# Performance work log

Hardware: AMD Instinct MI355X
Metric: run time of the kernel (lower is better)

Reference implementation:

```python
import jax, jax.numpy as jnp
import numpy as np

SCALE = 8.0  # sqrt(head_dim=64)
B, H, S, D = 2, 16, 2048, 64


def setup_inputs() -> dict:
    key = jax.random.key(0)
    kq, kk, kv = jax.random.split(key, 3)
    query = jax.random.normal(kq, (B, H, S, D), dtype=jnp.float32)
    key_t = jax.random.normal(kk, (B, H, S, D), dtype=jnp.float32)
    value = jax.random.normal(kv, (B, H, S, D), dtype=jnp.float32)
    # causal target mask (B, 1, S, S); 0 = masked
    mask = jnp.broadcast_to(jnp.tril(jnp.ones((S, S), dtype=jnp.int32)), (B, 1, S, S))
    return {"query": query, "key": key_t, "value": value, "mask": mask}


def reference(query, key, value, mask):
    # scores: (B, H, S, S)
    scores = jnp.einsum("bhqd,bhkd->bhqk", query, key) / SCALE
    scores = jnp.where(mask == 0, -jnp.inf, scores)
    attn = jax.nn.softmax(scores, axis=-1)  # dropout_rate=0.0 -> identity
    return jnp.einsum("bhqk,bhkd->bhqd", attn, value)
```

## Files before the change

### kernel.cpp

```cpp
#include <hip/hip_runtime.h>
#include <hip/hip_bf16.h>


#define S_ 2048
#define D_ 64
#define NBH 32

typedef __bf16 bf16x8 __attribute__((ext_vector_type(8)));
typedef float f32x16 __attribute__((ext_vector_type(16)));
typedef unsigned short u16x4 __attribute__((ext_vector_type(4)));
typedef unsigned short u16x8 __attribute__((ext_vector_type(8)));
typedef unsigned int u32;
typedef u32 u32x4 __attribute__((ext_vector_type(4)));

static __device__ __forceinline__ unsigned short bfb(float f) {
    return __builtin_bit_cast(unsigned short, (__bf16)f);
}
static __device__ __forceinline__ u32 pk2(float lo, float hi) {
    return (u32)bfb(lo) | ((u32)bfb(hi) << 16);
}

__global__ __launch_bounds__(256)
void prep_kv(const float* __restrict__ K, const float* __restrict__ V,
             unsigned short* __restrict__ Kbf, unsigned short* __restrict__ Vt) {
    const int bh = blockIdx.x >> 5;
    const int kvbase = (blockIdx.x & 31) << 6;

    const float* Ks = K + (size_t)bh * S_ * D_ + (size_t)kvbase * D_;
    unsigned short* Kd = Kbf + (size_t)bh * S_ * D_ + (size_t)kvbase * D_;
    #pragma unroll
    for (int i = 0; i < 4; ++i) {
        const int p = i * 256 + threadIdx.x;
        float4 x = reinterpret_cast<const float4*>(Ks)[p];
        u16x4 o = { bfb(x.x), bfb(x.y), bfb(x.z), bfb(x.w) };
        reinterpret_cast<u16x4*>(Kd)[p] = o;
    }

    __shared__ float Vl[64][65];
    const float* Vb = V + (size_t)bh * S_ * D_ + (size_t)kvbase * D_;
    #pragma unroll
    for (int i = 0; i < 4; ++i) {
        const int flat = i * 1024 + threadIdx.x * 4;
        const int kv = flat >> 6, d = flat & 63;
        float4 x = *reinterpret_cast<const float4*>(Vb + kv * D_ + d);
        Vl[kv][d] = x.x; Vl[kv][d + 1] = x.y; Vl[kv][d + 2] = x.z; Vl[kv][d + 3] = x.w;
    }
    __syncthreads();
    unsigned short* Vo = Vt + (size_t)bh * D_ * S_;
    #pragma unroll
    for (int i = 0; i < 2; ++i) {
        const int p = i * 256 + threadIdx.x;
        const int d = p >> 3, c = p & 7;
        u16x8 o;
        #pragma unroll
        for (int j = 0; j < 8; ++j) o[j] = bfb(Vl[c * 8 + j][d]);
        *reinterpret_cast<u16x8*>(Vo + d * S_ + kvbase + c * 8) = o;
    }
}

#define MFMA32(a, b, c) __builtin_amdgcn_mfma_f32_32x32x16_bf16((a), (b), (c), 0, 0, 0)

__global__ __launch_bounds__(256, 2)
void attn_fwd6(const float* __restrict__ Q, const unsigned short* __restrict__ Kbf,
               const unsigned short* __restrict__ Vtbf, float* __restrict__ O) {
    const int tid  = threadIdx.x;
    const int wq   = tid >> 6;
    const int lane = tid & 63;
    const int lq   = lane & 31;
    const int hi   = lane >> 5;

    const int bid = blockIdx.x;
    const int bh  = bid & 31;
    const int jb  = 15 - (bid >> 5);
    const int q0w = jb * 128 + wq * 32;

    const int nkv_b = 2 * jb + 2;
    const int nkv_w = 2 * jb + 1 + (wq >> 1);

    const unsigned short* Kg = Kbf  + (size_t)bh * S_ * D_;
    const unsigned short* Vg = Vtbf + (size_t)bh * D_ * S_;

    __shared__ __align__(16) unsigned short Kl[2][4096];
    __shared__ __align__(16) unsigned short Vl[2][4096];

    const float qscale = 0.18033688011112042f;
    bf16x8 qf[4];
    {
        const float* qsrc = Q + ((size_t)bh * S_ + q0w + lq) * D_;
        #pragma unroll
        for (int ks = 0; ks < 4; ++ks) {
            const float* p = qsrc + ks * 16 + hi * 8;
            float4 x = *reinterpret_cast<const float4*>(p);
            float4 y = *reinterpret_cast<const float4*>(p + 4);
            union { unsigned short u[8]; bf16x8 v; } t;
            t.u[0] = bfb(x.x * qscale); t.u[1] = bfb(x.y * qscale);
            t.u[2] = bfb(x.z * qscale); t.u[3] = bfb(x.w * qscale);
            t.u[4] = bfb(y.x * qscale); t.u[5] = bfb(y.y * qscale);
            t.u[6] = bfb(y.z * qscale); t.u[7] = bfb(y.w * qscale);
            qf[ks] = t.v;
        }
    }

    bf16x8 ones;
    #pragma unroll
    for (int i = 0; i < 8; ++i) ones[i] = (__bf16)1.0f;

    const unsigned short* kSrc[2];
    const unsigned short* vSrc[2];
    #pragma unroll
    for (int i = 0; i < 2; ++i) {
        const int p = i * 256 + tid, row = p >> 3;
        const int sc = (p & 7) ^ (row & 7);
        kSrc[i] = Kg + row * 64 + sc * 8;
        vSrc[i] = Vg + (size_t)row * S_ + sc * 8;
    }
    auto stage = [&](int buf, int t) {
        #pragma unroll
        for (int i = 0; i < 2; ++i) {
            const int p = i * 256 + tid;
            __builtin_amdgcn_global_load_lds(
                (const __attribute__((address_space(1))) void*)(kSrc[i] + t * 4096),
                (__attribute__((address_space(3))) void*)&Kl[buf][p * 8], 16, 0, 0);
            __builtin_amdgcn_global_load_lds(
                (const __attribute__((address_space(1))) void*)(vSrc[i] + t * 64),
                (__attribute__((address_space(3))) void*)&Vl[buf][p * 8], 16, 0, 0);
        }
    };

    f32x16 oa0, oa1, ssum;
    #pragma unroll
    for (int r = 0; r < 16; ++r) { oa0[r] = 0.f; oa1[r] = 0.f; ssum[r] = 0.f; }
    float m_ = -__builtin_inff();

    stage(0, 0);
    __syncthreads();

    for (int t = 0; t < nkv_b; ++t) {
        if (t + 1 < nkv_b) stage((t + 1) & 1, t + 1);
        if (t < nkv_w) {
            const unsigned short* Kb_ = Kl[t & 1];
            const unsigned short* Vb_ = Vl[t & 1];

            f32x16 s0, s1;
            #pragma unroll
            for (int r = 0; r < 16; ++r) { s0[r] = 0.f; s1[r] = 0.f; }
            __builtin_amdgcn_s_setprio(1);
            #pragma unroll
            for (int ks = 0; ks < 4; ++ks) {
                const int cc = 2 * ks + hi;
                bf16x8 k0 = *reinterpret_cast<const bf16x8*>(
                    &Kb_[((lq)*8      + (cc ^ (lq & 7))) * 8]);
                bf16x8 k1 = *reinterpret_cast<const bf16x8*>(
                    &Kb_[((32 + lq)*8 + (cc ^ (lq & 7))) * 8]);
                s0 = MFMA32(k0, qf[ks], s0);
                s1 = MFMA32(k1, qf[ks], s1);
            }
            __builtin_amdgcn_s_setprio(0);

            if (t == nkv_w - 1) {
                const int qg = q0w + lq - t * 64;
                #pragma unroll
                for (int r = 0; r < 16; ++r) {
                    const int kv0 = (r & 3) + 8 * (r >> 2) + 4 * hi;
                    if (kv0 > qg)      s0[r] = -__builtin_inff();
                    if (kv0 + 32 > qg) s1[r] = -__builtin_inff();
                }
            }

            float v = s0[0];
            #pragma unroll
            for (int r = 1; r < 16; ++r) v = fmaxf(v, s0[r]);
            #pragma unroll
            for (int r = 0; r < 16; ++r) v = fmaxf(v, s1[r]);
            v = fmaxf(v, __shfl_xor(v, 32));

            if (__any(v > m_ + 8.0f ? 1 : 0)) {
                const float mn = fmaxf(m_, v);
                const float al = __builtin_amdgcn_exp2f(m_ - mn);
                m_ = mn;
                ssum[0] *= al;
                #pragma unroll
                for (int r = 0; r < 16; ++r) { oa0[r] *= al; oa1[r] *= al; }
            }
            #pragma unroll
            for (int r = 0; r < 16; ++r) {
                s0[r] = __builtin_amdgcn_exp2f(s0[r] - m_);
                s1[r] = __builtin_amdgcn_exp2f(s1[r] - m_);
            }

            u32 c0[4][2], c1[4][2];
            #pragma unroll
            for (int tq = 0; tq < 4; ++tq) {
                c0[tq][0] = pk2(s0[4*tq+0], s0[4*tq+1]);
                c0[tq][1] = pk2(s0[4*tq+2], s0[4*tq+3]);
                c1[tq][0] = pk2(s1[4*tq+0], s1[4*tq+1]);
                c1[tq][1] = pk2(s1[4*tq+2], s1[4*tq+3]);
            }

            __builtin_amdgcn_s_setprio(1);
#define PVSTEP(KS, C, TL) { \
            u32 a0 = C[TL][0], a1 = C[TL][1], b0 = C[TL+1][0], b1 = C[TL+1][1]; \
            asm volatile("v_permlane32_swap_b32 %0, %1" : "+v"(a0), "+v"(b0)); \
            asm volatile("v_permlane32_swap_b32 %0, %1" : "+v"(a1), "+v"(b1)); \
            u32x4 w = { a0, a1, b0, b1 }; \
            bf16x8 pf = __builtin_bit_cast(bf16x8, w); \
            const int cc = 2*(KS) + hi; \
            bf16x8 v0 = *reinterpret_cast<const bf16x8*>( \
                &Vb_[((lq)*8      + (cc ^ (lq & 7))) * 8]); \
            bf16x8 v1 = *reinterpret_cast<const bf16x8*>( \
                &Vb_[((32 + lq)*8 + (cc ^ (lq & 7))) * 8]); \
            oa0 = MFMA32(v0, pf, oa0); \
            oa1 = MFMA32(v1, pf, oa1); \
            ssum = MFMA32(ones, pf, ssum); }
            PVSTEP(0, c0, 0) PVSTEP(1, c0, 2) PVSTEP(2, c1, 0) PVSTEP(3, c1, 2)
#undef PVSTEP
            __builtin_amdgcn_s_setprio(0);
        }
        __syncthreads();
    }

    const float inv = 1.0f / ssum[0];
    float* Ob = O + ((size_t)bh * S_ + q0w + lq) * D_;
    #pragma unroll
    for (int g = 0; g < 4; ++g) {
        float4 o0 = { oa0[4*g+0]*inv, oa0[4*g+1]*inv, oa0[4*g+2]*inv, oa0[4*g+3]*inv };
        *reinterpret_cast<float4*>(&Ob[8*g + 4*hi]) = o0;
        float4 o1 = { oa1[4*g+0]*inv, oa1[4*g+1]*inv, oa1[4*g+2]*inv, oa1[4*g+3]*inv };
        *reinterpret_cast<float4*>(&Ob[32 + 8*g + 4*hi]) = o1;
    }
}

extern "C" void kernel_launch(void* const* d_in, const int* in_sizes, int n_in,
                              void* d_out, int out_size, void* d_ws, size_t ws_size,
                              hipStream_t stream) {
    const float* Q = (const float*)d_in[0];
    const float* K = (const float*)d_in[1];
    const float* V = (const float*)d_in[2];
    float* O = (float*)d_out;

    unsigned short* Kbf = (unsigned short*)d_ws;
    unsigned short* Vt  = Kbf + (size_t)NBH * S_ * D_;

    hipLaunchKernelGGL(prep_kv,   dim3(1024), dim3(256), 0, stream, K, V, Kbf, Vt);
    hipLaunchKernelGGL(attn_fwd6, dim3(512),  dim3(256), 0, stream, Q, Kbf, Vt, O);
}
```

Before: 152.5 us.

## Split causal KV range across two blocks and merge partial outputs

Each query block's causal KV range is split into two halves processed by separate blocks (1024 blocks instead of 512). Each half writes unnormalized partial outputs plus its running max and sum. A new combine kernel then merges the halves with log-sum-exp weights. The aim is to shorten the critical path set by the longest diagonal blocks and to balance load across CUs. The cost is extra global traffic for the partial outputs, the stats and an extra launch. The original kernel remains as a fallback when the workspace is too small.

```diff
diff --git a/kernel.cpp b/kernel.cpp
--- a/kernel.cpp
+++ b/kernel.cpp
@@ -60,77 +60,211 @@
 
 #define MFMA32(a, b, c) __builtin_amdgcn_mfma_f32_32x32x16_bf16((a), (b), (c), 0, 0, 0)
 
+#define TILE_BODY(Kb_, Vb_, doMask, qg_expr)                                     \
+    {                                                                            \
+        f32x16 s0, s1;                                                           \
+        _Pragma("unroll")                                                        \
+        for (int r = 0; r < 16; ++r) { s0[r] = 0.f; s1[r] = 0.f; }               \
+        __builtin_amdgcn_s_setprio(1);                                           \
+        _Pragma("unroll")                                                        \
+        for (int ks = 0; ks < 4; ++ks) {                                         \
+            const int cc = 2 * ks + hi;                                          \
+            bf16x8 k0 = *reinterpret_cast<const bf16x8*>(                        \
+                &Kb_[((lq)*8      + (cc ^ (lq & 7))) * 8]);                      \
+            bf16x8 k1 = *reinterpret_cast<const bf16x8*>(                        \
+                &Kb_[((32 + lq)*8 + (cc ^ (lq & 7))) * 8]);                      \
+            s0 = MFMA32(k0, qf[ks], s0);                                         \
+            s1 = MFMA32(k1, qf[ks], s1);                                         \
+        }                                                                        \
+        __builtin_amdgcn_s_setprio(0);                                           \
+        if (doMask) {                                                            \
+            const int qg = (qg_expr);                                            \
+            _Pragma("unroll")                                                    \
+            for (int r = 0; r < 16; ++r) {                                       \
+                const int kv0 = (r & 3) + 8 * (r >> 2) + 4 * hi;                 \
+                if (kv0 > qg)      s0[r] = -__builtin_inff();                    \
+                if (kv0 + 32 > qg) s1[r] = -__builtin_inff();                    \
+            }                                                                    \
+        }                                                                        \
+        float v = s0[0];                                                         \
+        _Pragma("unroll")                                                        \
+        for (int r = 1; r < 16; ++r) v = fmaxf(v, s0[r]);                        \
+        _Pragma("unroll")                                                        \
+        for (int r = 0; r < 16; ++r) v = fmaxf(v, s1[r]);                        \
+        v = fmaxf(v, __shfl_xor(v, 32));                                         \
+        if (__any(v > m_ + 8.0f ? 1 : 0)) {                                      \
+            const float mn = fmaxf(m_, v);                                       \
+            const float al = __builtin_amdgcn_exp2f(m_ - mn);                    \
+            m_ = mn;                                                             \
+            ssum[0] *= al;                                                       \
+            _Pragma("unroll")                                                    \
+            for (int r = 0; r < 16; ++r) { oa0[r] *= al; oa1[r] *= al; }         \
+        }                                                                        \
+        _Pragma("unroll")                                                        \
+        for (int r = 0; r < 16; ++r) {                                           \
+            s0[r] = __builtin_amdgcn_exp2f(s0[r] - m_);                          \
+            s1[r] = __builtin_amdgcn_exp2f(s1[r] - m_);                          \
+        }                                                                        \
+        u32 c0[4][2], c1[4][2];                                                  \
+        _Pragma("unroll")                                                        \
+        for (int tq = 0; tq < 4; ++tq) {                                         \
+            c0[tq][0] = pk2(s0[4*tq+0], s0[4*tq+1]);                             \
+            c0[tq][1] = pk2(s0[4*tq+2], s0[4*tq+3]);                             \
+            c1[tq][0] = pk2(s1[4*tq+0], s1[4*tq+1]);                             \
+            c1[tq][1] = pk2(s1[4*tq+2], s1[4*tq+3]);                             \
+        }                                                                        \
+        __builtin_amdgcn_s_setprio(1);                                           \
+        PVSTEP(0, c0, 0) PVSTEP(1, c0, 2) PVSTEP(2, c1, 0) PVSTEP(3, c1, 2)      \
+        __builtin_amdgcn_s_setprio(0);                                           \
+    }
+
+#define PVSTEP(KS, C, TL) {                                                      \
+    u32 a0 = C[TL][0], a1 = C[TL][1], b0 = C[TL+1][0], b1 = C[TL+1][1];          \
+    asm volatile("v_permlane32_swap_b32 %0, %1" : "+v"(a0), "+v"(b0));           \
+    asm volatile("v_permlane32_swap_b32 %0, %1" : "+v"(a1), "+v"(b1));           \
+    u32x4 w = { a0, a1, b0, b1 };                                                \
+    bf16x8 pf = __builtin_bit_cast(bf16x8, w);                                   \
+    const int cc = 2*(KS) + hi;                                                  \
+    bf16x8 v0 = *reinterpret_cast<const bf16x8*>(                                \
+        &Vb_[((lq)*8      + (cc ^ (lq & 7))) * 8]);                              \
+    bf16x8 v1 = *reinterpret_cast<const bf16x8*>(                                \
+        &Vb_[((32 + lq)*8 + (cc ^ (lq & 7))) * 8]);                              \
+    oa0 = MFMA32(v0, pf, oa0);                                                   \
+    oa1 = MFMA32(v1, pf, oa1);                                                   \
+    ssum = MFMA32(ones, pf, ssum); }
+
+#define ATTN_PROLOGUE(Q0W_EXPR)                                                  \
+    const int tid  = threadIdx.x;                                                \
+    const int wq   = tid >> 6;                                                   \
+    const int lane = tid & 63;                                                   \
+    const int lq   = lane & 31;                                                  \
+    const int hi   = lane >> 5;                                                  \
+    const int q0w  = (Q0W_EXPR);                                                 \
+    const unsigned short* Kg = Kbf  + (size_t)bh * S_ * D_;                      \
+    const unsigned short* Vg = Vtbf + (size_t)bh * D_ * S_;                      \
+    const float qscale = 0.18033688011112042f;                                   \
+    bf16x8 qf[4];                                                                \
+    {                                                                            \
+        const float* qsrc = Q + ((size_t)bh * S_ + q0w + lq) * D_;               \
+        _Pragma("unroll")                                                        \
+        for (int ks = 0; ks < 4; ++ks) {                                         \
+            const float* p = qsrc + ks * 16 + hi * 8;                            \
+            float4 x = *reinterpret_cast<const float4*>(p);                      \
+            float4 y = *reinterpret_cast<const float4*>(p + 4);                  \
+            union { unsigned short u[8]; bf16x8 v; } tt;                         \
+            tt.u[0] = bfb(x.x * qscale); tt.u[1] = bfb(x.y * qscale);            \
+            tt.u[2] = bfb(x.z * qscale); tt.u[3] = bfb(x.w * qscale);            \
+            tt.u[4] = bfb(y.x * qscale); tt.u[5] = bfb(y.y * qscale);            \
+            tt.u[6] = bfb(y.z * qscale); tt.u[7] = bfb(y.w * qscale);            \
+            qf[ks] = tt.v;                                                       \
+        }                                                                        \
+    }                                                                            \
+    bf16x8 ones;                                                                 \
+    _Pragma("unroll")                                                            \
+    for (int i = 0; i < 8; ++i) ones[i] = (__bf16)1.0f;                          \
+    const unsigned short* kSrc[2];                                               \
+    const unsigned short* vSrc[2];                                               \
+    _Pragma("unroll")                                                            \
+    for (int i = 0; i < 2; ++i) {                                                \
+        const int p = i * 256 + tid, row = p >> 3;                               \
+        const int sc = (p & 7) ^ (row & 7);                                      \
+        kSrc[i] = Kg + row * 64 + sc * 8;                                        \
+        vSrc[i] = Vg + (size_t)row * S_ + sc * 8;                                \
+    }                                                                            \
+    auto stage = [&](int buf, int t) {                                           \
+        _Pragma("unroll")                                                        \
+        for (int i = 0; i < 2; ++i) {                                            \
+            const int p = i * 256 + tid;                                         \
+            __builtin_amdgcn_global_load_lds(                                    \
+                (const __attribute__((address_space(1))) void*)(kSrc[i] + t * 4096), \
+                (__attribute__((address_space(3))) void*)&Kl[buf][p * 8], 16, 0, 0); \
+            __builtin_amdgcn_global_load_lds(                                    \
+                (const __attribute__((address_space(1))) void*)(vSrc[i] + t * 64),   \
+                (__attribute__((address_space(3))) void*)&Vl[buf][p * 8], 16, 0, 0); \
+        }                                                                        \
+    };                                                                           \
+    f32x16 oa0, oa1, ssum;                                                       \
+    _Pragma("unroll")                                                            \
+    for (int r = 0; r < 16; ++r) { oa0[r] = 0.f; oa1[r] = 0.f; ssum[r] = 0.f; }  \
+    float m_ = -__builtin_inff();
+
+__global__ __launch_bounds__(256, 2)
+void attn_split(const float* __restrict__ Q, const unsigned short* __restrict__ Kbf,
+                const unsigned short* __restrict__ Vtbf,
+                float* __restrict__ OA, float* __restrict__ OB,
+                float* __restrict__ stats) {
+    const int bid  = blockIdx.x;
+    const int jb   = 15 - (bid >> 6);
+    const int half = (bid >> 5) & 1;
+    const int bh   = bid & 31;
+
+    __shared__ __align__(16) unsigned short Kl[2][4096];
+    __shared__ __align__(16) unsigned short Vl[2][4096];
+
+    ATTN_PROLOGUE(jb * 128 + wq * 32)
+
+    const int t0   = half ? (jb + 1) : 0;
+    const int tEnd = half ? (2 * jb + 2) : (jb + 1);
+    const int nkv_w = 2 * jb + 1 + (wq >> 1);
+
+    stage(t0 & 1, t0);
+    __syncthreads();
+
+    for (int t = t0; t < tEnd; ++t) {
+        if (t + 1 < tEnd) stage((t + 1) & 1, t + 1);
+        if (t < nkv_w) {
+            const unsigned short* Kb_ = Kl[t & 1];
+            const unsigned short* Vb_ = Vl[t & 1];
+            TILE_BODY(Kb_, Vb_, (t == nkv_w - 1), q0w + lq - t * 64)
+        }
+        __syncthreads();
+    }
+
+    float* dst = (half ? OB : OA) + ((size_t)bh * S_ + q0w + lq) * D_;
+    #pragma unroll
+    for (int g = 0; g < 4; ++g) {
+        float4 o0 = { oa0[4*g+0], oa0[4*g+1], oa0[4*g+2], oa0[4*g+3] };
+        *reinterpret_cast<float4*>(&dst[8*g + 4*hi]) = o0;
+        float4 o1 = { oa1[4*g+0], oa1[4*g+1], oa1[4*g+2], oa1[4*g+3] };
+        *reinterpret_cast<float4*>(&dst[32 + 8*g + 4*hi]) = o1;
+    }
+    if (hi == 0) {
+        float* st = stats + (((size_t)bh << 11) + q0w + lq) * 4 + (half ? 2 : 0);
+        st[0] = m_;
+        st[1] = ssum[0];
+    }
+}
+
+__global__ __launch_bounds__(256)
+void combine(float* __restrict__ OA, const float* __restrict__ OB,
+             const float4* __restrict__ stats) {
+    const int p = blockIdx.x * 256 + threadIdx.x;
+    const float4 s = stats[p >> 4];
+    const float m  = fmaxf(s.x, s.z);
+    const float wA = __builtin_amdgcn_exp2f(s.x - m);
+    const float wB = __builtin_amdgcn_exp2f(s.z - m);
+    const float inv = 1.0f / (s.y * wA + s.w * wB);
+    float4 a = reinterpret_cast<float4*>(OA)[p];
+    float4 b = reinterpret_cast<const float4*>(OB)[p];
+    float4 o = { (a.x * wA + b.x * wB) * inv, (a.y * wA + b.y * wB) * inv,
+                 (a.z * wA + b.z * wB) * inv, (a.w * wA + b.w * wB) * inv };
+    reinterpret_cast<float4*>(OA)[p] = o;
+}
+
 __global__ __launch_bounds__(256, 2)
 void attn_fwd6(const float* __restrict__ Q, const unsigned short* __restrict__ Kbf,
                const unsigned short* __restrict__ Vtbf, float* __restrict__ O) {
-    const int tid  = threadIdx.x;
-    const int wq   = tid >> 6;
-    const int lane = tid & 63;
-    const int lq   = lane & 31;
-    const int hi   = lane >> 5;
-
     const int bid = blockIdx.x;
     const int bh  = bid & 31;
     const int jb  = 15 - (bid >> 5);
-    const int q0w = jb * 128 + wq * 32;
+
+    __shared__ __align__(16) unsigned short Kl[2][4096];
+    __shared__ __align__(16) unsigned short Vl[2][4096];
+
+    ATTN_PROLOGUE(jb * 128 + wq * 32)
 
     const int nkv_b = 2 * jb + 2;
     const int nkv_w = 2 * jb + 1 + (wq >> 1);
-
-    const unsigned short* Kg = Kbf  + (size_t)bh * S_ * D_;
-    const unsigned short* Vg = Vtbf + (size_t)bh * D_ * S_;
-
-    __shared__ __align__(16) unsigned short Kl[2][4096];
-    __shared__ __align__(16) unsigned short Vl[2][4096];
-
-    const float qscale = 0.18033688011112042f;
-    bf16x8 qf[4];
-    {
-        const float* qsrc = Q + ((size_t)bh * S_ + q0w + lq) * D_;
-        #pragma unroll
-        for (int ks = 0; ks < 4; ++ks) {
-            const float* p = qsrc + ks * 16 + hi * 8;
-            float4 x = *reinterpret_cast<const float4*>(p);
-            float4 y = *reinterpret_cast<const float4*>(p + 4);
-            union { unsigned short u[8]; bf16x8 v; } t;
-            t.u[0] = bfb(x.x * qscale); t.u[1] = bfb(x.y * qscale);
-            t.u[2] = bfb(x.z * qscale); t.u[3] = bfb(x.w * qscale);
-            t.u[4] = bfb(y.x * qscale); t.u[5] = bfb(y.y * qscale);
-            t.u[6] = bfb(y.z * qscale); t.u[7] = bfb(y.w * qscale);
-            qf[ks] = t.v;
-        }
-    }
-
-    bf16x8 ones;
-    #pragma unroll
-    for (int i = 0; i < 8; ++i) ones[i] = (__bf16)1.0f;
-
-    const unsigned short* kSrc[2];
-    const unsigned short* vSrc[2];
-    #pragma unroll
-    for (int i = 0; i < 2; ++i) {
-        const int p = i * 256 + tid, row = p >> 3;
-        const int sc = (p & 7) ^ (row & 7);
-        kSrc[i] = Kg + row * 64 + sc * 8;
-        vSrc[i] = Vg + (size_t)row * S_ + sc * 8;
-    }
-    auto stage = [&](int buf, int t) {
-        #pragma unroll
-        for (int i = 0; i < 2; ++i) {
-            const int p = i * 256 + tid;
-            __builtin_amdgcn_global_load_lds(
-                (const __attribute__((address_space(1))) void*)(kSrc[i] + t * 4096),
-                (__attribute__((address_space(3))) void*)&Kl[buf][p * 8], 16, 0, 0);
-            __builtin_amdgcn_global_load_lds(
-                (const __attribute__((address_space(1))) void*)(vSrc[i] + t * 64),
-                (__attribute__((address_space(3))) void*)&Vl[buf][p * 8], 16, 0, 0);
-        }
-    };
-
-    f32x16 oa0, oa1, ssum;
-    #pragma unroll
-    for (int r = 0; r < 16; ++r) { oa0[r] = 0.f; oa1[r] = 0.f; ssum[r] = 0.f; }
-    float m_ = -__builtin_inff();
 
     stage(0, 0);
     __syncthreads();
@@ -140,81 +274,7 @@
         if (t < nkv_w) {
             const unsigned short* Kb_ = Kl[t & 1];
             const unsigned short* Vb_ = Vl[t & 1];
-
-            f32x16 s0, s1;
-            #pragma unroll
-            for (int r = 0; r < 16; ++r) { s0[r] = 0.f; s1[r] = 0.f; }
-            __builtin_amdgcn_s_setprio(1);
-            #pragma unroll
-            for (int ks = 0; ks < 4; ++ks) {
-                const int cc = 2 * ks + hi;
-                bf16x8 k0 = *reinterpret_cast<const bf16x8*>(
-                    &Kb_[((lq)*8      + (cc ^ (lq & 7))) * 8]);
-                bf16x8 k1 = *reinterpret_cast<const bf16x8*>(
-                    &Kb_[((32 + lq)*8 + (cc ^ (lq & 7))) * 8]);
-                s0 = MFMA32(k0, qf[ks], s0);
-                s1 = MFMA32(k1, qf[ks], s1);
-            }
-            __builtin_amdgcn_s_setprio(0);
-
-            if (t == nkv_w - 1) {
-                const int qg = q0w + lq - t * 64;
-                #pragma unroll
-                for (int r = 0; r < 16; ++r) {
-                    const int kv0 = (r & 3) + 8 * (r >> 2) + 4 * hi;
-                    if (kv0 > qg)      s0[r] = -__builtin_inff();
-                    if (kv0 + 32 > qg) s1[r] = -__builtin_inff();
-                }
-            }
-
-            float v = s0[0];
-            #pragma unroll
-            for (int r = 1; r < 16; ++r) v = fmaxf(v, s0[r]);
-            #pragma unroll
-            for (int r = 0; r < 16; ++r) v = fmaxf(v, s1[r]);
-            v = fmaxf(v, __shfl_xor(v, 32));
-
-            if (__any(v > m_ + 8.0f ? 1 : 0)) {
-                const float mn = fmaxf(m_, v);
-                const float al = __builtin_amdgcn_exp2f(m_ - mn);
-                m_ = mn;
-                ssum[0] *= al;
-                #pragma unroll
-                for (int r = 0; r < 16; ++r) { oa0[r] *= al; oa1[r] *= al; }
-            }
-            #pragma unroll
-            for (int r = 0; r < 16; ++r) {
-                s0[r] = __builtin_amdgcn_exp2f(s0[r] - m_);
-                s1[r] = __builtin_amdgcn_exp2f(s1[r] - m_);
-            }
-
-            u32 c0[4][2], c1[4][2];
-            #pragma unroll
-            for (int tq = 0; tq < 4; ++tq) {
-                c0[tq][0] = pk2(s0[4*tq+0], s0[4*tq+1]);
-                c0[tq][1] = pk2(s0[4*tq+2], s0[4*tq+3]);
-                c1[tq][0] = pk2(s1[4*tq+0], s1[4*tq+1]);
-                c1[tq][1] = pk2(s1[4*tq+2], s1[4*tq+3]);
-            }
-
-            __builtin_amdgcn_s_setprio(1);
-#define PVSTEP(KS, C, TL) { \
-            u32 a0 = C[TL][0], a1 = C[TL][1], b0 = C[TL+1][0], b1 = C[TL+1][1]; \
-            asm volatile("v_permlane32_swap_b32 %0, %1" : "+v"(a0), "+v"(b0)); \
-            asm volatile("v_permlane32_swap_b32 %0, %1" : "+v"(a1), "+v"(b1)); \
-            u32x4 w = { a0, a1, b0, b1 }; \
-            bf16x8 pf = __builtin_bit_cast(bf16x8, w); \
-            const int cc = 2*(KS) + hi; \
-            bf16x8 v0 = *reinterpret_cast<const bf16x8*>( \
-                &Vb_[((lq)*8      + (cc ^ (lq & 7))) * 8]); \
-            bf16x8 v1 = *reinterpret_cast<const bf16x8*>( \
-                &Vb_[((32 + lq)*8 + (cc ^ (lq & 7))) * 8]); \
-            oa0 = MFMA32(v0, pf, oa0); \
-            oa1 = MFMA32(v1, pf, oa1); \
-            ssum = MFMA32(ones, pf, ssum); }
-            PVSTEP(0, c0, 0) PVSTEP(1, c0, 2) PVSTEP(2, c1, 0) PVSTEP(3, c1, 2)
-#undef PVSTEP
-            __builtin_amdgcn_s_setprio(0);
+            TILE_BODY(Kb_, Vb_, (t == nkv_w - 1), q0w + lq - t * 64)
         }
         __syncthreads();
     }
@@ -241,6 +301,20 @@
     unsigned short* Kbf = (unsigned short*)d_ws;
     unsigned short* Vt  = Kbf + (size_t)NBH * S_ * D_;
 
-    hipLaunchKernelGGL(prep_kv,   dim3(1024), dim3(256), 0, stream, K, V, Kbf, Vt);
-    hipLaunchKernelGGL(attn_fwd6, dim3(512),  dim3(256), 0, stream, Q, Kbf, Vt, O);
-}
+    hipLaunchKernelGGL(prep_kv, dim3(1024), dim3(256), 0, stream, K, V, Kbf, Vt);
+
+    const size_t needed = (size_t)NBH * S_ * D_ * 2 * 2
+                        + (size_t)NBH * S_ * D_ * 4
+                        + (size_t)NBH * S_ * 16;
+    if (ws_size >= needed) {
+        float* OB    = (float*)(Vt + (size_t)NBH * S_ * D_);
+        float* stats = OB + (size_t)NBH * S_ * D_;
+        hipLaunchKernelGGL(attn_split, dim3(1024), dim3(256), 24576, stream,
+                           Q, Kbf, Vt, O, OB, stats);
+        hipLaunchKernelGGL(combine, dim3(4096), dim3(256), 0, stream,
+                           O, OB, (const float4*)stats);
+    } else {
+        hipLaunchKernelGGL(attn_fwd6, dim3(512), dim3(256), 0, stream,
+                           Q, Kbf, Vt, O);
+    }
+}
```

New measurement: 153.0 us. No clear change (+0.3%).

## Pre-swizzle K/V into MFMA fragment layout and load per-wave from global, dropping LDS

Applied to the files above, without the earlier changes.

The prep kernel now writes K and V in bf16 directly in the per-lane MFMA operand order, so each wave in the attention kernel loads its fragments straight from global memory into registers. This removes LDS staging and block-wide barriers. Each wave becomes an independent 32-row query strip, with causal load balancing done by pairing long and short strips across waves. The row sum is now computed with VALU reductions instead of an extra ones-MFMA. The cost is that each wave re-reads K/V from global or L2 without sharing across the block, which raises L2 traffic and register pressure.

```diff
diff --git a/kernel.cpp b/kernel.cpp
--- a/kernel.cpp
+++ b/kernel.cpp
@@ -8,7 +8,6 @@
 
 typedef __bf16 bf16x8 __attribute__((ext_vector_type(8)));
 typedef float f32x16 __attribute__((ext_vector_type(16)));
-typedef unsigned short u16x4 __attribute__((ext_vector_type(4)));
 typedef unsigned short u16x8 __attribute__((ext_vector_type(8)));
 typedef unsigned int u32;
 typedef u32 u32x4 __attribute__((ext_vector_type(4)));
@@ -21,67 +20,81 @@
 }
 
 __global__ __launch_bounds__(256)
-void prep_kv(const float* __restrict__ K, const float* __restrict__ V,
-             unsigned short* __restrict__ Kbf, unsigned short* __restrict__ Vt) {
+void prep_frag(const float* __restrict__ K, const float* __restrict__ V,
+               unsigned short* __restrict__ Kf, unsigned short* __restrict__ Vf) {
     const int bh = blockIdx.x >> 5;
-    const int kvbase = (blockIdx.x & 31) << 6;
-
-    const float* Ks = K + (size_t)bh * S_ * D_ + (size_t)kvbase * D_;
-    unsigned short* Kd = Kbf + (size_t)bh * S_ * D_ + (size_t)kvbase * D_;
-    #pragma unroll
-    for (int i = 0; i < 4; ++i) {
-        const int p = i * 256 + threadIdx.x;
-        float4 x = reinterpret_cast<const float4*>(Ks)[p];
-        u16x4 o = { bfb(x.x), bfb(x.y), bfb(x.z), bfb(x.w) };
-        reinterpret_cast<u16x4*>(Kd)[p] = o;
-    }
-
-    __shared__ float Vl[64][65];
-    const float* Vb = V + (size_t)bh * S_ * D_ + (size_t)kvbase * D_;
+    const int t  = blockIdx.x & 31;
+    __shared__ float Ka[64][65];
+    __shared__ float Va[64][65];
+    const float* Ks = K + ((size_t)bh * S_ + t * 64) * D_;
+    const float* Vs = V + ((size_t)bh * S_ + t * 64) * D_;
     #pragma unroll
     for (int i = 0; i < 4; ++i) {
         const int flat = i * 1024 + threadIdx.x * 4;
-        const int kv = flat >> 6, d = flat & 63;
-        float4 x = *reinterpret_cast<const float4*>(Vb + kv * D_ + d);
-        Vl[kv][d] = x.x; Vl[kv][d + 1] = x.y; Vl[kv][d + 2] = x.z; Vl[kv][d + 3] = x.w;
+        const int s = flat >> 6, d = flat & 63;
+        float4 kx = *reinterpret_cast<const float4*>(Ks + s * D_ + d);
+        Ka[s][d] = kx.x; Ka[s][d+1] = kx.y; Ka[s][d+2] = kx.z; Ka[s][d+3] = kx.w;
+        float4 vx = *reinterpret_cast<const float4*>(Vs + s * D_ + d);
+        Va[s][d] = vx.x; Va[s][d+1] = vx.y; Va[s][d+2] = vx.z; Va[s][d+3] = vx.w;
     }
     __syncthreads();
-    unsigned short* Vo = Vt + (size_t)bh * D_ * S_;
+    const size_t tb = ((size_t)bh * 32 + t) * 512;
     #pragma unroll
     for (int i = 0; i < 2; ++i) {
-        const int p = i * 256 + threadIdx.x;
-        const int d = p >> 3, c = p & 7;
-        u16x8 o;
-        #pragma unroll
-        for (int j = 0; j < 8; ++j) o[j] = bfb(Vl[c * 8 + j][d]);
-        *reinterpret_cast<u16x8*>(Vo + d * S_ + kvbase + c * 8) = o;
+        const int u  = i * 256 + threadIdx.x;
+        const int h  = u >> 8, ks = (u >> 6) & 3, h2 = (u >> 5) & 1, l2 = u & 31;
+        const int d0 = 8 * (2 * ks + h2);
+        u16x8 ok, ov;
+        #pragma unroll
+        for (int j = 0; j < 8; ++j) {
+            ok[j] = bfb(Ka[h * 32 + l2][d0 + j]);
+            ov[j] = bfb(Va[d0 + j][h * 32 + l2]);
+        }
+        *reinterpret_cast<u16x8*>(Kf + (tb + u) * 8) = ok;
+        *reinterpret_cast<u16x8*>(Vf + (tb + u) * 8) = ov;
     }
 }
 
 #define MFMA32(a, b, c) __builtin_amdgcn_mfma_f32_32x32x16_bf16((a), (b), (c), 0, 0, 0)
 
+#define LOADF(DST, BASE, T) { \
+    const unsigned short* fb_ = (BASE) + (size_t)(T) * 4096 + lane * 8; \
+    DST[0] = *reinterpret_cast<const bf16x8*>(fb_); \
+    DST[1] = *reinterpret_cast<const bf16x8*>(fb_ + 512); \
+    DST[2] = *reinterpret_cast<const bf16x8*>(fb_ + 1024); \
+    DST[3] = *reinterpret_cast<const bf16x8*>(fb_ + 1536); \
+    DST[4] = *reinterpret_cast<const bf16x8*>(fb_ + 2048); \
+    DST[5] = *reinterpret_cast<const bf16x8*>(fb_ + 2560); \
+    DST[6] = *reinterpret_cast<const bf16x8*>(fb_ + 3072); \
+    DST[7] = *reinterpret_cast<const bf16x8*>(fb_ + 3584); }
+
+#define PVSTEP(KS, C, TL) { \
+    u32 a0 = C[TL][0], a1 = C[TL][1], b0 = C[TL+1][0], b1 = C[TL+1][1]; \
+    asm volatile("v_permlane32_swap_b32 %0, %1" : "+v"(a0), "+v"(b0)); \
+    asm volatile("v_permlane32_swap_b32 %0, %1" : "+v"(a1), "+v"(b1)); \
+    u32x4 w = { a0, a1, b0, b1 }; \
+    bf16x8 pf = __builtin_bit_cast(bf16x8, w); \
+    oa0 = MFMA32(vA[KS],     pf, oa0); \
+    oa1 = MFMA32(vA[4 + KS], pf, oa1); }
+
 __global__ __launch_bounds__(256, 2)
-void attn_fwd6(const float* __restrict__ Q, const unsigned short* __restrict__ Kbf,
-               const unsigned short* __restrict__ Vtbf, float* __restrict__ O) {
+void attn_frag(const float* __restrict__ Q, const unsigned short* __restrict__ Kf,
+               const unsigned short* __restrict__ Vf, float* __restrict__ O) {
     const int tid  = threadIdx.x;
     const int wq   = tid >> 6;
     const int lane = tid & 63;
     const int lq   = lane & 31;
     const int hi   = lane >> 5;
 
-    const int bid = blockIdx.x;
-    const int bh  = bid & 31;
-    const int jb  = 15 - (bid >> 5);
-    const int q0w = jb * 128 + wq * 32;
-
-    const int nkv_b = 2 * jb + 2;
-    const int nkv_w = 2 * jb + 1 + (wq >> 1);
-
-    const unsigned short* Kg = Kbf  + (size_t)bh * S_ * D_;
-    const unsigned short* Vg = Vtbf + (size_t)bh * D_ * S_;
-
-    __shared__ __align__(16) unsigned short Kl[2][4096];
-    __shared__ __align__(16) unsigned short Vl[2][4096];
+    const int wid = blockIdx.x * 4 + wq;
+    int qs, bh;
+    if (wid < 1024) { qs = 63 - (wid >> 5); bh = wid & 31; }
+    else            { qs = (wid - 1024) >> 5; bh = (wid - 1024) & 31; }
+    const int q0w = qs * 32;
+    const int nt  = (qs >> 1) + 1;
+
+    const unsigned short* Kg = Kf + (size_t)bh * 131072;
+    const unsigned short* Vg = Vf + (size_t)bh * 131072;
 
     const float qscale = 0.18033688011112042f;
     bf16x8 qf[4];
@@ -92,134 +105,98 @@
             const float* p = qsrc + ks * 16 + hi * 8;
             float4 x = *reinterpret_cast<const float4*>(p);
             float4 y = *reinterpret_cast<const float4*>(p + 4);
-            union { unsigned short u[8]; bf16x8 v; } t;
-            t.u[0] = bfb(x.x * qscale); t.u[1] = bfb(x.y * qscale);
-            t.u[2] = bfb(x.z * qscale); t.u[3] = bfb(x.w * qscale);
-            t.u[4] = bfb(y.x * qscale); t.u[5] = bfb(y.y * qscale);
-            t.u[6] = bfb(y.z * qscale); t.u[7] = bfb(y.w * qscale);
-            qf[ks] = t.v;
-        }
-    }
-
-    bf16x8 ones;
-    #pragma unroll
-    for (int i = 0; i < 8; ++i) ones[i] = (__bf16)1.0f;
-
-    const unsigned short* kSrc[2];
-    const unsigned short* vSrc[2];
-    #pragma unroll
-    for (int i = 0; i < 2; ++i) {
-        const int p = i * 256 + tid, row = p >> 3;
-        const int sc = (p & 7) ^ (row & 7);
-        kSrc[i] = Kg + row * 64 + sc * 8;
-        vSrc[i] = Vg + (size_t)row * S_ + sc * 8;
-    }
-    auto stage = [&](int buf, int t) {
-        #pragma unroll
-        for (int i = 0; i < 2; ++i) {
-            const int p = i * 256 + tid;
-            __builtin_amdgcn_global_load_lds(
-                (const __attribute__((address_space(1))) void*)(kSrc[i] + t * 4096),
-                (__attribute__((address_space(3))) void*)&Kl[buf][p * 8], 16, 0, 0);
-            __builtin_amdgcn_global_load_lds(
-                (const __attribute__((address_space(1))) void*)(vSrc[i] + t * 64),
-                (__attribute__((address_space(3))) void*)&Vl[buf][p * 8], 16, 0, 0);
-        }
-    };
-
-    f32x16 oa0, oa1, ssum;
-    #pragma unroll
-    for (int r = 0; r < 16; ++r) { oa0[r] = 0.f; oa1[r] = 0.f; ssum[r] = 0.f; }
-    float m_ = -__builtin_inff();
-
-    stage(0, 0);
-    __syncthreads();
-
-    for (int t = 0; t < nkv_b; ++t) {
-        if (t + 1 < nkv_b) stage((t + 1) & 1, t + 1);
-        if (t < nkv_w) {
-            const unsigned short* Kb_ = Kl[t & 1];
-            const unsigned short* Vb_ = Vl[t & 1];
-
-            f32x16 s0, s1;
-            #pragma unroll
-            for (int r = 0; r < 16; ++r) { s0[r] = 0.f; s1[r] = 0.f; }
-            __builtin_amdgcn_s_setprio(1);
-            #pragma unroll
-            for (int ks = 0; ks < 4; ++ks) {
-                const int cc = 2 * ks + hi;
-                bf16x8 k0 = *reinterpret_cast<const bf16x8*>(
-                    &Kb_[((lq)*8      + (cc ^ (lq & 7))) * 8]);
-                bf16x8 k1 = *reinterpret_cast<const bf16x8*>(
-                    &Kb_[((32 + lq)*8 + (cc ^ (lq & 7))) * 8]);
-                s0 = MFMA32(k0, qf[ks], s0);
-                s1 = MFMA32(k1, qf[ks], s1);
+            union { unsigned short u[8]; bf16x8 v; } tt;
+            tt.u[0] = bfb(x.x * qscale); tt.u[1] = bfb(x.y * qscale);
+            tt.u[2] = bfb(x.z * qscale); tt.u[3] = bfb(x.w * qscale);
+            tt.u[4] = bfb(y.x * qscale); tt.u[5] = bfb(y.y * qscale);
+            tt.u[6] = bfb(y.z * qscale); tt.u[7] = bfb(y.w * qscale);
+            qf[ks] = tt.v;
+        }
+    }
+
+    f32x16 oa0, oa1;
+    #pragma unroll
+    for (int r = 0; r < 16; ++r) { oa0[r] = 0.f; oa1[r] = 0.f; }
+    float m_ = -__builtin_inff(), l_ = 0.f;
+
+    bf16x8 kA[8], vA[8];
+    LOADF(kA, Kg, 0)
+    LOADF(vA, Vg, 0)
+
+    for (int t = 0; t < nt; ++t) {
+        const int tn = (t + 1 < 32) ? (t + 1) : 31;
+
+        f32x16 s0, s1;
+        #pragma unroll
+        for (int r = 0; r < 16; ++r) { s0[r] = 0.f; s1[r] = 0.f; }
+        __builtin_amdgcn_s_setprio(1);
+        #pragma unroll
+        for (int ks = 0; ks < 4; ++ks) {
+            s0 = MFMA32(kA[ks],     qf[ks], s0);
+            s1 = MFMA32(kA[4 + ks], qf[ks], s1);
+        }
+        __builtin_amdgcn_s_setprio(0);
+
+        LOADF(kA, Kg, tn)
+
+        if (t == nt - 1) {
+            const int qg = q0w + lq - t * 64;
+            #pragma unroll
+            for (int r = 0; r < 16; ++r) {
+                const int kv0 = (r & 3) + 8 * (r >> 2) + 4 * hi;
+                if (kv0 > qg)      s0[r] = -__builtin_inff();
+                if (kv0 + 32 > qg) s1[r] = -__builtin_inff();
             }
-            __builtin_amdgcn_s_setprio(0);
-
-            if (t == nkv_w - 1) {
-                const int qg = q0w + lq - t * 64;
-                #pragma unroll
-                for (int r = 0; r < 16; ++r) {
-                    const int kv0 = (r & 3) + 8 * (r >> 2) + 4 * hi;
-                    if (kv0 > qg)      s0[r] = -__builtin_inff();
-                    if (kv0 + 32 > qg) s1[r] = -__builtin_inff();
-                }
-            }
-
-            float v = s0[0];
-            #pragma unroll
-            for (int r = 1; r < 16; ++r) v = fmaxf(v, s0[r]);
-            #pragma unroll
-            for (int r = 0; r < 16; ++r) v = fmaxf(v, s1[r]);
-            v = fmaxf(v, __shfl_xor(v, 32));
-
-            if (__any(v > m_ + 8.0f ? 1 : 0)) {
-                const float mn = fmaxf(m_, v);
-                const float al = __builtin_amdgcn_exp2f(m_ - mn);
-                m_ = mn;
-                ssum[0] *= al;
-                #pragma unroll
-                for (int r = 0; r < 16; ++r) { oa0[r] *= al; oa1[r] *= al; }
-            }
-            #pragma unroll
-            for (int r = 0; r < 16; ++r) {
-                s0[r] = __builtin_amdgcn_exp2f(s0[r] - m_);
-                s1[r] = __builtin_amdgcn_exp2f(s1[r] - m_);
-            }
-
-            u32 c0[4][2], c1[4][2];
-            #pragma unroll
-            for (int tq = 0; tq < 4; ++tq) {
-                c0[tq][0] = pk2(s0[4*tq+0], s0[4*tq+1]);
-                c0[tq][1] = pk2(s0[4*tq+2], s0[4*tq+3]);
-                c1[tq][0] = pk2(s1[4*tq+0], s1[4*tq+1]);
-                c1[tq][1] = pk2(s1[4*tq+2], s1[4*tq+3]);
-            }
-
-            __builtin_amdgcn_s_setprio(1);
-#define PVSTEP(KS, C, TL) { \
-            u32 a0 = C[TL][0], a1 = C[TL][1], b0 = C[TL+1][0], b1 = C[TL+1][1]; \
-            asm volatile("v_permlane32_swap_b32 %0, %1" : "+v"(a0), "+v"(b0)); \
-            asm volatile("v_permlane32_swap_b32 %0, %1" : "+v"(a1), "+v"(b1)); \
-            u32x4 w = { a0, a1, b0, b1 }; \
-            bf16x8 pf = __builtin_bit_cast(bf16x8, w); \
-            const int cc = 2*(KS) + hi; \
-            bf16x8 v0 = *reinterpret_cast<const bf16x8*>( \
-                &Vb_[((lq)*8      + (cc ^ (lq & 7))) * 8]); \
-            bf16x8 v1 = *reinterpret_cast<const bf16x8*>( \
-                &Vb_[((32 + lq)*8 + (cc ^ (lq & 7))) * 8]); \
-            oa0 = MFMA32(v0, pf, oa0); \
-            oa1 = MFMA32(v1, pf, oa1); \
-            ssum = MFMA32(ones, pf, ssum); }
-            PVSTEP(0, c0, 0) PVSTEP(1, c0, 2) PVSTEP(2, c1, 0) PVSTEP(3, c1, 2)
-#undef PVSTEP
-            __builtin_amdgcn_s_setprio(0);
-        }
-        __syncthreads();
-    }
-
-    const float inv = 1.0f / ssum[0];
+        }
+
+        float mx[16];
+        #pragma unroll
+        for (int r = 0; r < 16; ++r) mx[r] = fmaxf(s0[r], s1[r]);
+        #pragma unroll
+        for (int off = 8; off >= 1; off >>= 1)
+            for (int r = 0; r < off; ++r) mx[r] = fmaxf(mx[r], mx[r + off]);
+        const float v = fmaxf(mx[0], __shfl_xor(mx[0], 32));
+        if (__any(v > m_ + 8.0f ? 1 : 0)) {
+            const float mn = fmaxf(m_, v);
+            const float al = __builtin_amdgcn_exp2f(m_ - mn);
+            m_ = mn;
+            l_ *= al;
+            #pragma unroll
+            for (int r = 0; r < 16; ++r) { oa0[r] *= al; oa1[r] *= al; }
+        }
+        #pragma unroll
+        for (int r = 0; r < 16; ++r) {
+            s0[r] = __builtin_amdgcn_exp2f(s0[r] - m_);
+            s1[r] = __builtin_amdgcn_exp2f(s1[r] - m_);
+        }
+
+        {
+            float ts[16];
+            #pragma unroll
+            for (int r = 0; r < 16; ++r) ts[r] = s0[r] + s1[r];
+            #pragma unroll
+            for (int off = 8; off >= 1; off >>= 1)
+                for (int r = 0; r < off; ++r) ts[r] += ts[r + off];
+            l_ += ts[0] + __shfl_xor(ts[0], 32);
+        }
+
+        u32 c0[4][2], c1[4][2];
+        #pragma unroll
+        for (int tq = 0; tq < 4; ++tq) {
+            c0[tq][0] = pk2(s0[4*tq+0], s0[4*tq+1]);
+            c0[tq][1] = pk2(s0[4*tq+2], s0[4*tq+3]);
+            c1[tq][0] = pk2(s1[4*tq+0], s1[4*tq+1]);
+            c1[tq][1] = pk2(s1[4*tq+2], s1[4*tq+3]);
+        }
+
+        __builtin_amdgcn_s_setprio(1);
+        PVSTEP(0, c0, 0) PVSTEP(1, c0, 2) PVSTEP(2, c1, 0) PVSTEP(3, c1, 2)
+        __builtin_amdgcn_s_setprio(0);
+
+        LOADF(vA, Vg, tn)
+    }
+
+    const float inv = 1.0f / l_;
     float* Ob = O + ((size_t)bh * S_ + q0w + lq) * D_;
     #pragma unroll
     for (int g = 0; g < 4; ++g) {
@@ -238,9 +215,9 @@
     const float* V = (const float*)d_in[2];
     float* O = (float*)d_out;
 
-    unsigned short* Kbf = (unsigned short*)d_ws;
-    unsigned short* Vt  = Kbf + (size_t)NBH * S_ * D_;
-
-    hipLaunchKernelGGL(prep_kv,   dim3(1024), dim3(256), 0, stream, K, V, Kbf, Vt);
-    hipLaunchKernelGGL(attn_fwd6, dim3(512),  dim3(256), 0, stream, Q, Kbf, Vt, O);
-}
+    unsigned short* Kf = (unsigned short*)d_ws;
+    unsigned short* Vf = Kf + (size_t)4194304;
+
+    hipLaunchKernelGGL(prep_frag, dim3(1024), dim3(256), 0, stream, K, V, Kf, Vf);
+    hipLaunchKernelGGL(attn_frag, dim3(512),  dim3(256), 0, stream, Q, Kf, Vf, O);
+}
```

Result: faster. 139.7 us (-8.4%).
